# Performance work log

Hardware: AMD Instinct MI355X
Metric: run time of the kernel (lower is better)

## Reference

```python
import jax, jax.numpy as jnp
import numpy as np

N_NODES = 100000
N_TYPES = 7
N_EDGES = 400000
D = 128


def setup_inputs() -> dict:
    key = jax.random.key(0)
    k1, k2, k3, k4 = jax.random.split(key, 4)
    x = jax.random.normal(k1, (N_NODES, D), dtype=jnp.float32)
    edge_indices = jax.random.randint(k2, (N_TYPES, 2, N_EDGES), 0, N_NODES, dtype=jnp.int64)
    # per-type linear weights of the cloned base GNNs (scaled for stability)
    W = jax.random.normal(k3, (N_TYPES, D, D), dtype=jnp.float32) * (1.0 / np.sqrt(D))
    b = jax.random.normal(k4, (N_TYPES, D), dtype=jnp.float32) * 0.02
    return {"x": x, "edge_indices": edge_indices, "W": W, "b": b}


def _type_conv(x, src, dst, Wt, bt, n_nodes):
    # gather -> segment-mean aggregate -> linear, one edge type
    msg = x[src]                                                   # [E, D]
    summed = jax.ops.segment_sum(msg, dst, num_segments=n_nodes)   # [N, D]
    cnt = jax.ops.segment_sum(jnp.ones(src.shape, x.dtype), dst, num_segments=n_nodes)
    mean = summed / jnp.maximum(cnt, 1.0)[:, None]
    return mean @ Wt + bt


def reference(x, edge_indices, W, b):
    n_nodes = x.shape[0]
    n_types = edge_indices.shape[0]
    # loop over the small fixed set of edge types (structurally distinct GNNs)
    acc = jnp.zeros_like(x)
    for t in range(n_types):
        acc = acc + _type_conv(x, edge_indices[t, 0], edge_indices[t, 1], W[t], b[t], n_nodes)
    return acc / n_types
```

## Files before the change

kernel.cpp:

```cpp
#include <hip/hip_runtime.h>

#define N_NODES 100000
#define N_TYPES 7
#define N_EDGES 400000
#define DIM 128
#define NTOT (N_TYPES * N_NODES)
#define ETOT (N_TYPES * N_EDGES)

#define RBITS 10
#define RNODE 1024
#define NBUCK 98
#define BSTRIDE 128
#define CAP 6144
#define CHUNK 2048
#define NCHUNKS ((N_EDGES + CHUNK - 1) / CHUNK)

typedef short v8s __attribute__((ext_vector_type(8)));
typedef float v4f __attribute__((ext_vector_type(4)));

__device__ __forceinline__ unsigned short f2bf(float f) {
    unsigned int x = __float_as_uint(f);
    return (unsigned short)((x + 0x7FFFu + ((x >> 16) & 1u)) >> 16);
}

__global__ __launch_bounds__(256) void cast_x_kernel(
    const float* __restrict__ x, unsigned short* __restrict__ xb)
{
    int i = blockIdx.x * 256 + threadIdx.x;
    if (i >= N_NODES * DIM / 4) return;
    float4 v = reinterpret_cast<const float4*>(x)[i];
    ushort4 o;
    o.x = f2bf(v.x); o.y = f2bf(v.y); o.z = f2bf(v.z); o.w = f2bf(v.w);
    reinterpret_cast<ushort4*>(xb)[i] = o;
}

__global__ __launch_bounds__(256) void cast_wt_kernel(
    const float* __restrict__ W, unsigned short* __restrict__ WT)
{
    int i = blockIdx.x * 256 + threadIdx.x;
    if (i >= N_TYPES * DIM * DIM) return;
    int t = i >> 14, r = i & 16383, j = r >> 7, k = r & 127;
    WT[i] = f2bf(W[(t << 14) + (k << 7) + j]);
}

__global__ __launch_bounds__(128) void bsum_kernel(
    const float* __restrict__ b, float* __restrict__ bsum)
{
    int j = threadIdx.x;
    float s = 0.f;
    for (int t = 0; t < N_TYPES; ++t) s += b[t * DIM + j];
    bsum[j] = s;
}

__global__ __launch_bounds__(256) void binpass_kernel(
    const int* __restrict__ ei, int* __restrict__ gcur,
    unsigned int* __restrict__ bucketbuf)
{
    __shared__ unsigned int packedLds[CHUNK];
    __shared__ unsigned char bLds[CHUNK];
    __shared__ unsigned int sortedLds[CHUNK];
    __shared__ int cnt[BSTRIDE];
    __shared__ int lofs[BSTRIDE];
    __shared__ int gbase[BSTRIDE];

    const int blk = blockIdx.x;
    const int t = blk / NCHUNKS;
    const int c = blk - t * NCHUNKS;
    const int* srcp = ei + (size_t)t * 2 * N_EDGES;
    const int* dstp = srcp + N_EDGES;
    const int e0 = c * CHUNK;
    const int e1 = min(e0 + CHUNK, N_EDGES);
    const int tid = threadIdx.x;

    if (tid < BSTRIDE) cnt[tid] = 0;
    __syncthreads();

#pragma unroll
    for (int k = 0; k < CHUNK / 256; ++k) {
        int j = tid + k * 256;
        int e = e0 + j;
        unsigned char b = 0xFF;
        unsigned int pk = 0;
        if (e < e1) {
            int s = srcp[e];
            int d = dstp[e];
            b = (unsigned char)(d >> RBITS);
            pk = ((unsigned int)(d & (RNODE - 1)) << 17) | (unsigned int)s;
            atomicAdd(&cnt[b], 1);
        }
        packedLds[j] = pk;
        bLds[j] = b;
    }
    __syncthreads();

    if (tid < BSTRIDE) lofs[tid] = cnt[tid];
    __syncthreads();
    for (int off = 1; off < BSTRIDE; off <<= 1) {
        int tv = 0;
        if (tid >= off && tid < BSTRIDE) tv = lofs[tid - off];
        __syncthreads();
        if (tid < BSTRIDE) lofs[tid] += tv;
        __syncthreads();
    }
    if (tid < BSTRIDE) lofs[tid] -= cnt[tid];
    __syncthreads();

    if (tid < BSTRIDE) {
        int n = cnt[tid];
        int base = -1;
        if (n > 0 && tid < NBUCK) {
            int rel = atomicAdd(&gcur[t * BSTRIDE + tid], n);
            base = (t * BSTRIDE + tid) * CAP + rel;
        }
        gbase[tid] = base;
        cnt[tid] = lofs[tid];
    }
    __syncthreads();

#pragma unroll
    for (int k = 0; k < CHUNK / 256; ++k) {
        int j = tid + k * 256;
        unsigned char b = bLds[j];
        if (b != 0xFF) {
            int p = atomicAdd(&cnt[b], 1);
            sortedLds[p] = packedLds[j];
        }
    }
    __syncthreads();

    const int wave = tid >> 6, lane = tid & 63;
    for (int b = wave * 32; b < wave * 32 + 32; ++b) {
        if (b >= NBUCK) break;
        int base = gbase[b];
        if (base < 0) continue;
        int o = lofs[b];
        int n = cnt[b] - o;
        for (int i = lane; i < n; i += 64)
            bucketbuf[(size_t)base + i] = sortedLds[o + i];
    }
}

__global__ __launch_bounds__(256) void bucket_hist_kernel(
    const unsigned int* __restrict__ bucketbuf, const int* __restrict__ gcur,
    int* __restrict__ deg)
{
    __shared__ int cnt[RNODE];
    const int blk = blockIdx.x;
    const int t = blk / NBUCK;
    const int b = blk - t * NBUCK;
    const int n = min(gcur[t * BSTRIDE + b], CAP);
    const int g0 = b << RBITS;
    const int validR = min(RNODE, N_NODES - g0);
    const int tid = threadIdx.x;
    for (int j = tid; j < RNODE; j += 256) cnt[j] = 0;
    __syncthreads();
    const unsigned int* bb = bucketbuf + (size_t)(t * BSTRIDE + b) * CAP;
    for (int i = tid; i < n; i += 256)
        atomicAdd(&cnt[bb[i] >> 17], 1);
    __syncthreads();
    int* dg = deg + (size_t)t * N_NODES + g0;
    for (int j = tid; j < validR; j += 256) dg[j] = cnt[j];
}

__global__ __launch_bounds__(256) void scan1_kernel(
    const int* __restrict__ deg, int* __restrict__ offs, int* __restrict__ bsum)
{
    __shared__ int s[256];
    int tid = threadIdx.x;
    int base = blockIdx.x * 1024 + tid * 4;
    int v[4];
    int tot = 0;
#pragma unroll
    for (int j = 0; j < 4; ++j) {
        v[j] = (base + j < NTOT) ? deg[base + j] : 0;
        tot += v[j];
    }
    s[tid] = tot;
    __syncthreads();
    for (int off = 1; off < 256; off <<= 1) {
        int t2 = (tid >= off) ? s[tid - off] : 0;
        __syncthreads();
        s[tid] += t2;
        __syncthreads();
    }
    if (tid == 255) bsum[blockIdx.x] = s[255];
    int run = s[tid] - tot;
#pragma unroll
    for (int j = 0; j < 4; ++j) {
        if (base + j < NTOT) offs[base + j] = run;
        run += v[j];
    }
}

__global__ __launch_bounds__(1024) void scan2_kernel(int* __restrict__ bsum, int nb)
{
    __shared__ int s[1024];
    int tid = threadIdx.x;
    int v = (tid < nb) ? bsum[tid] : 0;
    s[tid] = v;
    __syncthreads();
    for (int off = 1; off < 1024; off <<= 1) {
        int t2 = (tid >= off) ? s[tid - off] : 0;
        __syncthreads();
        s[tid] += t2;
        __syncthreads();
    }
    if (tid < nb) bsum[tid] = s[tid] - v;
}

__global__ __launch_bounds__(256) void scan3_kernel(
    int* __restrict__ offs, const int* __restrict__ bsum)
{
    int i = blockIdx.x * 256 + threadIdx.x;
    if (i < NTOT) offs[i] += bsum[i >> 10];
    if (i == 0) offs[NTOT] = ETOT;
}

__global__ __launch_bounds__(256) void place_kernel(
    const unsigned int* __restrict__ bucketbuf, const int* __restrict__ gcur,
    const int* __restrict__ offs, int* __restrict__ srcperm)
{
    __shared__ int cur[RNODE];
    __shared__ int sorted[CAP];
    const int blk = blockIdx.x;
    const int t = blk / NBUCK;
    const int b = blk - t * NBUCK;
    const int n = min(gcur[t * BSTRIDE + b], CAP);
    const int g0 = b << RBITS;
    const int validR = min(RNODE, N_NODES - g0);
    const int tid = threadIdx.x;
    const int* offt = offs + (size_t)t * N_NODES + g0;
    const int base0 = offt[0];
    for (int j = tid; j < validR; j += 256) cur[j] = offt[j] - base0;
    __syncthreads();
    const unsigned int* bb = bucketbuf + (size_t)(t * BSTRIDE + b) * CAP;
    for (int i = tid; i < n; i += 256) {
        unsigned int pk = bb[i];
        int p = atomicAdd(&cur[pk >> 17], 1);
        sorted[p] = (int)(pk & 0x1FFFFu);
    }
    __syncthreads();
    int* outp = srcperm + base0;
    for (int i = tid; i < n; i += 256) outp[i] = sorted[i];
}

__global__ __launch_bounds__(256) void aggregate_kernel(
    const unsigned short* __restrict__ xb,
    const int* __restrict__ offs,
    const int* __restrict__ srcperm,
    unsigned short* __restrict__ meanout,
    int grp0, int ngrp)
{
    int gi = blockIdx.x * 16 + (threadIdx.x >> 4);
    if (gi >= ngrp) return;
    int grp = grp0 + gi;
    int l = threadIdx.x & 15;

    int beg = offs[grp];
    int end = offs[grp + 1];
    int m = end - beg;

    int mm = m;
    mm = max(mm, __shfl_xor(mm, 16));
    mm = max(mm, __shfl_xor(mm, 32));

    float a[8];
#pragma unroll
    for (int j = 0; j < 8; ++j) a[j] = 0.f;

    const int eSafe = min(beg, ETOT - 1);
#pragma unroll 2
    for (int i = 0; i < mm; ++i) {
        bool valid = i < m;
        int e = valid ? (beg + i) : eSafe;
        int s = srcperm[e];
        uint4 v = *reinterpret_cast<const uint4*>(
            reinterpret_cast<const char*>(xb) + ((size_t)s << 8) + (l << 4));
        float w = valid ? 1.f : 0.f;
        a[0] += w * __uint_as_float(v.x << 16);
        a[1] += w * __uint_as_float(v.x & 0xFFFF0000u);
        a[2] += w * __uint_as_float(v.y << 16);
        a[3] += w * __uint_as_float(v.y & 0xFFFF0000u);
        a[4] += w * __uint_as_float(v.z << 16);
        a[5] += w * __uint_as_float(v.z & 0xFFFF0000u);
        a[6] += w * __uint_as_float(v.w << 16);
        a[7] += w * __uint_as_float(v.w & 0xFFFF0000u);
    }

    float inv = 1.0f / fmaxf((float)m, 1.0f);
    unsigned int p0, p1, p2, p3;
    asm("v_cvt_pk_bf16_f32 %0, %1, %2" : "=v"(p0) : "v"(a[0] * inv), "v"(a[1] * inv));
    asm("v_cvt_pk_bf16_f32 %0, %1, %2" : "=v"(p1) : "v"(a[2] * inv), "v"(a[3] * inv));
    asm("v_cvt_pk_bf16_f32 %0, %1, %2" : "=v"(p2) : "v"(a[4] * inv), "v"(a[5] * inv));
    asm("v_cvt_pk_bf16_f32 %0, %1, %2" : "=v"(p3) : "v"(a[6] * inv), "v"(a[7] * inv));
    uint4 o = make_uint4(p0, p1, p2, p3);
    *reinterpret_cast<uint4*>(
        reinterpret_cast<char*>(meanout) + ((size_t)gi << 8) + (l << 4)) = o;
}

__global__ __launch_bounds__(256) void matmul_kernel(
    const unsigned short* __restrict__ meanall, size_t meanStride,
    int t0, int nt,
    const unsigned short* __restrict__ WT,
    const float* __restrict__ bsum,
    float* __restrict__ out, int accum)
{
    __shared__ unsigned short sB[DIM * DIM];

    const int tid = threadIdx.x;
    const int wave = tid >> 6;
    const int lane = tid & 63;
    const int rlo = lane & 15;
    const int khi = lane >> 4;
    const int row0 = blockIdx.x * 64 + wave * 16;

    v4f acc[8];
#pragma unroll
    for (int n = 0; n < 8; ++n) acc[n] = (v4f){0.f, 0.f, 0.f, 0.f};

    for (int tt = 0; tt < nt; ++tt) {
        int t = t0 + tt;
        __syncthreads();
        const uint4* gw = reinterpret_cast<const uint4*>(WT + ((size_t)t << 14));
#pragma unroll
        for (int i = 0; i < 8; ++i) {
            int c = tid + (i << 8);
            uint4 v = gw[c];
            int L = c << 4;
            int row = L >> 8;
            int sb = (row << 8) | ((L & 255) ^ ((row & 7) << 4));
            *reinterpret_cast<uint4*>(reinterpret_cast<char*>(sB) + sb) = v;
        }
        __syncthreads();

        int rowA = row0 + rlo;
        if (rowA >= N_NODES) rowA = N_NODES - 1;
        const unsigned short* arow = meanall + (size_t)tt * meanStride + ((size_t)rowA << 7);

#pragma unroll
        for (int k0 = 0; k0 < DIM; k0 += 32) {
            v8s a = *reinterpret_cast<const v8s*>(arow + k0 + (khi << 3));
#pragma unroll
            for (int n = 0; n < 8; ++n) {
                int jrow = (n << 4) | rlo;
                int kb = (k0 + (khi << 3)) << 1;
                int sb = (jrow << 8) | (kb ^ ((jrow & 7) << 4));
                v8s bf = *reinterpret_cast<const v8s*>(reinterpret_cast<char*>(sB) + sb);
                acc[n] = __builtin_amdgcn_mfma_f32_16x16x32_bf16(a, bf, acc[n], 0, 0, 0);
            }
        }
    }

    const float inv7 = 1.0f / 7.0f;
#pragma unroll
    for (int n = 0; n < 8; ++n) {
        int col = (n << 4) | rlo;
        float bs = bsum[col];
#pragma unroll
        for (int r = 0; r < 4; ++r) {
            int row = row0 + (khi << 2) + r;
            if (row < N_NODES) {
                float* p = out + ((size_t)row << 7) + col;
                if (accum) *p += acc[n][r] * inv7;
                else       *p = (acc[n][r] + bs) * inv7;
            }
        }
    }
}

__global__ __launch_bounds__(256) void out_init_kernel(
    const float* __restrict__ bsum, float* __restrict__ out)
{
    int i = blockIdx.x * 256 + threadIdx.x;
    if (i >= N_NODES * DIM / 4) return;
    int c4 = (i & 31) * 4;
    const float inv7 = 1.0f / 7.0f;
    float4 bv = *reinterpret_cast<const float4*>(bsum + c4);
    float4 o = make_float4(bv.x * inv7, bv.y * inv7, bv.z * inv7, bv.w * inv7);
    reinterpret_cast<float4*>(out)[i] = o;
}

extern "C" void kernel_launch(void* const* d_in, const int* in_sizes, int n_in,
                              void* d_out, int out_size, void* d_ws, size_t ws_size,
                              hipStream_t stream) {
    const float* x  = (const float*)d_in[0];
    const int*   ei = (const int*)d_in[1];
    const float* W  = (const float*)d_in[2];
    const float* b  = (const float*)d_in[3];
    float* out = (float*)d_out;

    char* p = (char*)d_ws;
    unsigned short* xb = (unsigned short*)p;          p += (size_t)N_NODES * DIM * 2;
    unsigned short* WT = (unsigned short*)p;          p += (size_t)N_TYPES * DIM * DIM * 2;
    float* bsum = (float*)p;                          p += 512;
    int* srcperm = (int*)p;                           p += (size_t)ETOT * 4;
    int* deg = (int*)p;                               p += (size_t)NTOT * 4;
    int* offs = (int*)p;                              p += (size_t)(NTOT + 1) * 4;
    int* bscan = (int*)p;                             p += 1024 * 4;
    int* gcur = (int*)p;                              p += (size_t)N_TYPES * BSTRIDE * 4;
    p = (char*)(((uintptr_t)p + 15) & ~(uintptr_t)15);
    unsigned short* meanbuf = (unsigned short*)p;
    unsigned int* bucketbuf = (unsigned int*)p;
    size_t mean1_bytes = (size_t)N_NODES * DIM * 2;
    size_t used = (size_t)(p - (char*)d_ws);
    bool fused = (ws_size >= used + 7 * mean1_bytes);

    const int NB = (NTOT + 1023) / 1024;

    cast_x_kernel<<<(N_NODES * DIM / 4 + 255) / 256, 256, 0, stream>>>(x, xb);
    cast_wt_kernel<<<(N_TYPES * DIM * DIM + 255) / 256, 256, 0, stream>>>(W, WT);
    bsum_kernel<<<1, 128, 0, stream>>>(b, bsum);

    hipMemsetAsync(gcur, 0, (size_t)N_TYPES * BSTRIDE * 4, stream);
    binpass_kernel<<<N_TYPES * NCHUNKS, 256, 0, stream>>>(ei, gcur, bucketbuf);
    bucket_hist_kernel<<<N_TYPES * NBUCK, 256, 0, stream>>>(bucketbuf, gcur, deg);
    scan1_kernel<<<NB, 256, 0, stream>>>(deg, offs, bscan);
    scan2_kernel<<<1, 1024, 0, stream>>>(bscan, NB);
    scan3_kernel<<<(NTOT + 255) / 256, 256, 0, stream>>>(offs, bscan);
    place_kernel<<<N_TYPES * NBUCK, 256, 0, stream>>>(bucketbuf, gcur, offs, srcperm);

    const int matmul_blocks = (N_NODES + 63) / 64;

    if (fused) {
        size_t meanStride = (size_t)N_NODES * DIM;
        aggregate_kernel<<<(NTOT + 15) / 16, 256, 0, stream>>>(
            xb, offs, srcperm, meanbuf, 0, NTOT);
        matmul_kernel<<<matmul_blocks, 256, 0, stream>>>(
            meanbuf, meanStride, 0, N_TYPES, WT, bsum, out, 0);
    } else {
        out_init_kernel<<<(N_NODES * DIM / 4 + 255) / 256, 256, 0, stream>>>(bsum, out);
        for (int t = 0; t < N_TYPES; ++t) {
            aggregate_kernel<<<(N_NODES + 15) / 16, 256, 0, stream>>>(
                xb, offs, srcperm, meanbuf, t * N_NODES, N_NODES);
            matmul_kernel<<<matmul_blocks, 256, 0, stream>>>(
                meanbuf, 0, t, 1, WT, bsum, out, 1);
        }
    }
}
```

Measured before the change: 250.0 us.

## Fuse neighbor aggregation and per-type matmul into one kernel via LDS

Replaces the separate aggregate and matmul kernels with one fused kernel. Each wave gathers and averages neighbor features for 16 nodes per edge type, writes the bf16 means to a swizzled LDS tile, and immediately runs the MFMA product against that type's weights, which are now read directly from global memory instead of staged in LDS. This removes the round trip of the 7x[N,128] bf16 mean buffer through HBM and a kernel launch. In exchange it cuts gather parallelism, since each wave now handles only 16 rows with 4 gathered rows per lane, and it reloads weights from global/L2 on every block.

```diff
diff --git a/kernel.cpp b/kernel.cpp
--- a/kernel.cpp
+++ b/kernel.cpp
@@ -244,109 +244,103 @@
     for (int i = tid; i < n; i += 256) outp[i] = sorted[i];
 }
 
-__global__ __launch_bounds__(256) void aggregate_kernel(
+__global__ __launch_bounds__(256, 4) void fused_kernel(
     const unsigned short* __restrict__ xb,
     const int* __restrict__ offs,
     const int* __restrict__ srcperm,
-    unsigned short* __restrict__ meanout,
-    int grp0, int ngrp)
-{
-    int gi = blockIdx.x * 16 + (threadIdx.x >> 4);
-    if (gi >= ngrp) return;
-    int grp = grp0 + gi;
-    int l = threadIdx.x & 15;
-
-    int beg = offs[grp];
-    int end = offs[grp + 1];
-    int m = end - beg;
-
-    int mm = m;
-    mm = max(mm, __shfl_xor(mm, 16));
-    mm = max(mm, __shfl_xor(mm, 32));
-
-    float a[8];
-#pragma unroll
-    for (int j = 0; j < 8; ++j) a[j] = 0.f;
-
-    const int eSafe = min(beg, ETOT - 1);
-#pragma unroll 2
-    for (int i = 0; i < mm; ++i) {
-        bool valid = i < m;
-        int e = valid ? (beg + i) : eSafe;
-        int s = srcperm[e];
-        uint4 v = *reinterpret_cast<const uint4*>(
-            reinterpret_cast<const char*>(xb) + ((size_t)s << 8) + (l << 4));
-        float w = valid ? 1.f : 0.f;
-        a[0] += w * __uint_as_float(v.x << 16);
-        a[1] += w * __uint_as_float(v.x & 0xFFFF0000u);
-        a[2] += w * __uint_as_float(v.y << 16);
-        a[3] += w * __uint_as_float(v.y & 0xFFFF0000u);
-        a[4] += w * __uint_as_float(v.z << 16);
-        a[5] += w * __uint_as_float(v.z & 0xFFFF0000u);
-        a[6] += w * __uint_as_float(v.w << 16);
-        a[7] += w * __uint_as_float(v.w & 0xFFFF0000u);
-    }
-
-    float inv = 1.0f / fmaxf((float)m, 1.0f);
-    unsigned int p0, p1, p2, p3;
-    asm("v_cvt_pk_bf16_f32 %0, %1, %2" : "=v"(p0) : "v"(a[0] * inv), "v"(a[1] * inv));
-    asm("v_cvt_pk_bf16_f32 %0, %1, %2" : "=v"(p1) : "v"(a[2] * inv), "v"(a[3] * inv));
-    asm("v_cvt_pk_bf16_f32 %0, %1, %2" : "=v"(p2) : "v"(a[4] * inv), "v"(a[5] * inv));
-    asm("v_cvt_pk_bf16_f32 %0, %1, %2" : "=v"(p3) : "v"(a[6] * inv), "v"(a[7] * inv));
-    uint4 o = make_uint4(p0, p1, p2, p3);
-    *reinterpret_cast<uint4*>(
-        reinterpret_cast<char*>(meanout) + ((size_t)gi << 8) + (l << 4)) = o;
-}
-
-__global__ __launch_bounds__(256) void matmul_kernel(
-    const unsigned short* __restrict__ meanall, size_t meanStride,
-    int t0, int nt,
     const unsigned short* __restrict__ WT,
     const float* __restrict__ bsum,
-    float* __restrict__ out, int accum)
-{
-    __shared__ unsigned short sB[DIM * DIM];
+    float* __restrict__ out)
+{
+    __shared__ unsigned short sA[4][16 * DIM];
 
     const int tid = threadIdx.x;
     const int wave = tid >> 6;
     const int lane = tid & 63;
+    const int l = lane & 15;
+    const int gw = lane >> 4;
+    const int khi = lane >> 4;
     const int rlo = lane & 15;
-    const int khi = lane >> 4;
-    const int row0 = blockIdx.x * 64 + wave * 16;
+    const int row0 = blockIdx.x * 64;
+    const int wrow0 = row0 + wave * 16;
+    unsigned short* myA = sA[wave];
 
     v4f acc[8];
 #pragma unroll
     for (int n = 0; n < 8; ++n) acc[n] = (v4f){0.f, 0.f, 0.f, 0.f};
 
-    for (int tt = 0; tt < nt; ++tt) {
-        int t = t0 + tt;
-        __syncthreads();
-        const uint4* gw = reinterpret_cast<const uint4*>(WT + ((size_t)t << 14));
-#pragma unroll
-        for (int i = 0; i < 8; ++i) {
-            int c = tid + (i << 8);
-            uint4 v = gw[c];
-            int L = c << 4;
-            int row = L >> 8;
-            int sb = (row << 8) | ((L & 255) ^ ((row & 7) << 4));
-            *reinterpret_cast<uint4*>(reinterpret_cast<char*>(sB) + sb) = v;
-        }
-        __syncthreads();
-
-        int rowA = row0 + rlo;
-        if (rowA >= N_NODES) rowA = N_NODES - 1;
-        const unsigned short* arow = meanall + (size_t)tt * meanStride + ((size_t)rowA << 7);
-
+    for (int t = 0; t < N_TYPES; ++t) {
+        int begs[4], ms[4];
+#pragma unroll
+        for (int i = 0; i < 4; ++i) {
+            int g = wrow0 + gw * 4 + i;
+            bool vld = g < N_NODES;
+            int grp = t * N_NODES + (vld ? g : 0);
+            int b0 = offs[grp];
+            int e0 = offs[grp + 1];
+            begs[i] = b0;
+            ms[i] = vld ? (e0 - b0) : 0;
+        }
+        int mm = max(max(ms[0], ms[1]), max(ms[2], ms[3]));
+
+        float a[4][8];
+#pragma unroll
+        for (int i = 0; i < 4; ++i)
+#pragma unroll
+            for (int j = 0; j < 8; ++j) a[i][j] = 0.f;
+
+        for (int it = 0; it < mm; ++it) {
+            uint4 v[4];
+            float w[4];
+#pragma unroll
+            for (int i = 0; i < 4; ++i) {
+                bool valid = it < ms[i];
+                int e = valid ? (begs[i] + it) : 0;
+                int s = srcperm[e];
+                v[i] = *reinterpret_cast<const uint4*>(
+                    reinterpret_cast<const char*>(xb) + ((size_t)s << 8) + (l << 4));
+                w[i] = valid ? 1.f : 0.f;
+            }
+#pragma unroll
+            for (int i = 0; i < 4; ++i) {
+                a[i][0] += w[i] * __uint_as_float(v[i].x << 16);
+                a[i][1] += w[i] * __uint_as_float(v[i].x & 0xFFFF0000u);
+                a[i][2] += w[i] * __uint_as_float(v[i].y << 16);
+                a[i][3] += w[i] * __uint_as_float(v[i].y & 0xFFFF0000u);
+                a[i][4] += w[i] * __uint_as_float(v[i].z << 16);
+                a[i][5] += w[i] * __uint_as_float(v[i].z & 0xFFFF0000u);
+                a[i][6] += w[i] * __uint_as_float(v[i].w << 16);
+                a[i][7] += w[i] * __uint_as_float(v[i].w & 0xFFFF0000u);
+            }
+        }
+
+#pragma unroll
+        for (int i = 0; i < 4; ++i) {
+            float inv = 1.0f / fmaxf((float)ms[i], 1.0f);
+            unsigned int p0, p1, p2, p3;
+            asm("v_cvt_pk_bf16_f32 %0, %1, %2" : "=v"(p0) : "v"(a[i][0] * inv), "v"(a[i][1] * inv));
+            asm("v_cvt_pk_bf16_f32 %0, %1, %2" : "=v"(p1) : "v"(a[i][2] * inv), "v"(a[i][3] * inv));
+            asm("v_cvt_pk_bf16_f32 %0, %1, %2" : "=v"(p2) : "v"(a[i][4] * inv), "v"(a[i][5] * inv));
+            asm("v_cvt_pk_bf16_f32 %0, %1, %2" : "=v"(p3) : "v"(a[i][6] * inv), "v"(a[i][7] * inv));
+            uint4 o = make_uint4(p0, p1, p2, p3);
+            int r = gw * 4 + i;
+            int byte = (r << 8) + ((l << 4) ^ ((r & 7) << 4));
+            *reinterpret_cast<uint4*>(reinterpret_cast<char*>(myA) + byte) = o;
+        }
+
+        const unsigned short* wt = WT + ((size_t)t << 14);
 #pragma unroll
         for (int k0 = 0; k0 < DIM; k0 += 32) {
-            v8s a = *reinterpret_cast<const v8s*>(arow + k0 + (khi << 3));
+            int colb = (k0 << 1) + (khi << 4);
+            int abyte = (rlo << 8) + (colb ^ ((rlo & 7) << 4));
+            v8s afr = *reinterpret_cast<const v8s*>(
+                reinterpret_cast<const char*>(myA) + abyte);
 #pragma unroll
             for (int n = 0; n < 8; ++n) {
-                int jrow = (n << 4) | rlo;
-                int kb = (k0 + (khi << 3)) << 1;
-                int sb = (jrow << 8) | (kb ^ ((jrow & 7) << 4));
-                v8s bf = *reinterpret_cast<const v8s*>(reinterpret_cast<char*>(sB) + sb);
-                acc[n] = __builtin_amdgcn_mfma_f32_16x16x32_bf16(a, bf, acc[n], 0, 0, 0);
+                int col = (n << 4) | rlo;
+                v8s bfr = *reinterpret_cast<const v8s*>(
+                    wt + (col << 7) + k0 + (khi << 3));
+                acc[n] = __builtin_amdgcn_mfma_f32_16x16x32_bf16(afr, bfr, acc[n], 0, 0, 0);
             }
         }
     }
@@ -358,26 +352,11 @@
         float bs = bsum[col];
 #pragma unroll
         for (int r = 0; r < 4; ++r) {
-            int row = row0 + (khi << 2) + r;
-            if (row < N_NODES) {
-                float* p = out + ((size_t)row << 7) + col;
-                if (accum) *p += acc[n][r] * inv7;
-                else       *p = (acc[n][r] + bs) * inv7;
-            }
-        }
-    }
-}
-
-__global__ __launch_bounds__(256) void out_init_kernel(
-    const float* __restrict__ bsum, float* __restrict__ out)
-{
-    int i = blockIdx.x * 256 + threadIdx.x;
-    if (i >= N_NODES * DIM / 4) return;
-    int c4 = (i & 31) * 4;
-    const float inv7 = 1.0f / 7.0f;
-    float4 bv = *reinterpret_cast<const float4*>(bsum + c4);
-    float4 o = make_float4(bv.x * inv7, bv.y * inv7, bv.z * inv7, bv.w * inv7);
-    reinterpret_cast<float4*>(out)[i] = o;
+            int row = wrow0 + (khi << 2) + r;
+            if (row < N_NODES)
+                out[((size_t)row << 7) + col] = (acc[n][r] + bs) * inv7;
+        }
+    }
 }
 
 extern "C" void kernel_launch(void* const* d_in, const int* in_sizes, int n_in,
@@ -399,11 +378,7 @@
     int* bscan = (int*)p;                             p += 1024 * 4;
     int* gcur = (int*)p;                              p += (size_t)N_TYPES * BSTRIDE * 4;
     p = (char*)(((uintptr_t)p + 15) & ~(uintptr_t)15);
-    unsigned short* meanbuf = (unsigned short*)p;
     unsigned int* bucketbuf = (unsigned int*)p;
-    size_t mean1_bytes = (size_t)N_NODES * DIM * 2;
-    size_t used = (size_t)(p - (char*)d_ws);
-    bool fused = (ws_size >= used + 7 * mean1_bytes);
 
     const int NB = (NTOT + 1023) / 1024;
 
@@ -419,21 +394,6 @@
     scan3_kernel<<<(NTOT + 255) / 256, 256, 0, stream>>>(offs, bscan);
     place_kernel<<<N_TYPES * NBUCK, 256, 0, stream>>>(bucketbuf, gcur, offs, srcperm);
 
-    const int matmul_blocks = (N_NODES + 63) / 64;
-
-    if (fused) {
-        size_t meanStride = (size_t)N_NODES * DIM;
-        aggregate_kernel<<<(NTOT + 15) / 16, 256, 0, stream>>>(
-            xb, offs, srcperm, meanbuf, 0, NTOT);
-        matmul_kernel<<<matmul_blocks, 256, 0, stream>>>(
-            meanbuf, meanStride, 0, N_TYPES, WT, bsum, out, 0);
-    } else {
-        out_init_kernel<<<(N_NODES * DIM / 4 + 255) / 256, 256, 0, stream>>>(bsum, out);
-        for (int t = 0; t < N_TYPES; ++t) {
-            aggregate_kernel<<<(N_NODES + 15) / 16, 256, 0, stream>>>(
-                xb, offs, srcperm, meanbuf, t * N_NODES, N_NODES);
-            matmul_kernel<<<matmul_blocks, 256, 0, stream>>>(
-                meanbuf, 0, t, 1, WT, bsum, out, 1);
-        }
-    }
-}
+    const int fused_blocks = (N_NODES + 63) / 64;
+    fused_kernel<<<fused_blocks, 256, 0, stream>>>(xb, offs, srcperm, WT, bsum, out);
+}
```

After: 361.2 us. 1.44x slower.
